# Performance work log

Hardware: AMD Instinct MI355X
Metric: run time of the kernel (lower is better)

## Reference

```python
import jax, jax.numpy as jnp
import numpy as np

EPS = 1e-5
TOPK = 4

def bn(x, gamma, beta, mean, var, axis=1):
    # inference-mode batchnorm (running stats)
    shp = [1] * x.ndim
    shp[axis] = -1
    scale = (gamma / jnp.sqrt(var + EPS)).reshape(shp)
    shift = (beta - mean * gamma / jnp.sqrt(var + EPS)).reshape(shp)
    return x * scale + shift


def setup_inputs() -> dict:
    key = jax.random.key(0)
    ks = jax.random.split(key, 4)
    B, C, T, H, W = 8, 512, 8, 28, 28
    R = 64
    Cq = C // 4
    s = 0.05
    return {
        "input": jax.random.normal(ks[0], (B, C, T, H, W), dtype=jnp.float32),
        "w_reduce": jax.random.normal(ks[1], (R, C), dtype=jnp.float32) * s,
        "bn1_gamma": jnp.ones((R,), jnp.float32), "bn1_beta": jnp.zeros((R,), jnp.float32),
        "bn1_mean": jnp.zeros((R,), jnp.float32), "bn1_var": jnp.ones((R,), jnp.float32),
        "w_proj": jax.random.normal(ks[2], (Cq, C + 2), dtype=jnp.float32) * s,
        "bn2_gamma": jnp.ones((Cq,), jnp.float32), "bn2_beta": jnp.zeros((Cq,), jnp.float32),
        "bn2_mean": jnp.zeros((Cq,), jnp.float32), "bn2_var": jnp.ones((Cq,), jnp.float32),
        "w_t": jax.random.normal(ks[3], (C, Cq, 3, 1), dtype=jnp.float32) * s,
        "bn3_gamma": jnp.ones((C,), jnp.float32), "bn3_beta": jnp.zeros((C,), jnp.float32),
        "bn3_mean": jnp.zeros((C,), jnp.float32), "bn3_var": jnp.ones((C,), jnp.float32),
    }


def reference(input, w_reduce, bn1_gamma, bn1_beta, bn1_mean, bn1_var,
              w_proj, bn2_gamma, bn2_beta, bn2_mean, bn2_var,
              w_t, bn3_gamma, bn3_beta, bn3_mean, bn3_var):
    x = input
    B, C, T, H, W = x.shape
    R = w_reduce.shape[0]
    K = TOPK
    HW = H * W

    # spatial template from frame 0
    template_d = x[:, :, 0].reshape(B, C, HW)                                  # (B,C,HW)
    template_p = bn(jnp.einsum('rc,bcs->brs', w_reduce, template_d),
                    bn1_gamma, bn1_beta, bn1_mean, bn1_var)                     # (B,R,HW)
    spt_inds = jnp.argmax(template_p, axis=2)                                  # (B,R)
    template_resample = jnp.take_along_axis(template_d, spt_inds[:, None, :], axis=2)  # (B,C,R)

    x_flat = x.reshape(B, C, T * HW)
    affinity = jnp.einsum('bcr,bcs->brs', template_resample, x_flat)           # (B,R,T*HW)
    affinity = affinity.reshape(B, R, T, HW)
    _, topk_inds = jax.lax.top_k(affinity, K)                                  # (B,R,T,K)
    inds = jnp.transpose(topk_inds, (0, 3, 2, 1))                              # (B,K,T,R)

    # gather trajectory features: traj[b,k,c,t,r] = x[b,c,t, inds[b,k,t,r]]
    x4 = x.reshape(B, C, T, HW)
    traj = jnp.take_along_axis(x4[:, None], inds[:, :, None], axis=4)          # (B,K,C,T,R)
    traj_bk = traj.reshape(B * K, C, T, R)

    inds_bk = inds.reshape(B * K, 1, T, R)
    row = (inds_bk // W).astype(jnp.float32) / H
    col = (inds_bk % W).astype(jnp.float32) / W
    coords = jnp.concatenate([row, col], axis=1)                               # (B*K,2,T,R)

    fuse = jnp.concatenate([traj_bk, coords], axis=1)                          # (B*K,C+2,T,R)
    fuse = bn(jnp.einsum('qc,bctr->bqtr', w_proj, fuse),
              bn2_gamma, bn2_beta, bn2_mean, bn2_var)                          # (B*K,C/4,T,R)
    fuse = fuse.reshape(B, K, C // 4, T, R).max(axis=1)                        # (B,C/4,T,R)

    tc = jax.lax.conv_general_dilated(fuse, w_t, window_strides=(1, 1),
                                      padding=((1, 1), (0, 0)),
                                      dimension_numbers=('NCHW', 'OIHW', 'NCHW'))
    tc = jax.nn.relu(bn(tc, bn3_gamma, bn3_beta, bn3_mean, bn3_var))           # (B,C,T,R)

    points = traj.mean(axis=1).reshape(B, C, T * R)                            # (B,C,T*R)
    proj = jnp.einsum('bcp,bcs->bps', points, x_flat)                          # (B,T*R,T*HW)
    proj = jax.nn.softmax(proj, axis=1)                                        # softmax over T*R (dim=1)
    prop = jnp.einsum('bcp,bps->bcs', tc.reshape(B, C, T * R), proj)           # (B,C,T*HW)
    return x + prop.reshape(B, C, T, H, W)
```

## Files before the change

### kernel.cpp

```cpp
#include <hip/hip_runtime.h>

#define EPSB 1e-5f

#define B_   8
#define C_   512
#define T_   8
#define HW_  784
#define S_   6272
#define R_   64
#define CQ_  128
#define K_   4
#define P_   512

typedef _Float16 f16;
typedef __attribute__((ext_vector_type(8))) _Float16 f16x8;
typedef __attribute__((ext_vector_type(4))) _Float16 f16x4;
typedef __attribute__((ext_vector_type(4))) float    f32x4;

#define OB_PTST  0ull
#define OB_TC    4194304ull
#define OB_D     8388608ull
#define OB_TRH   8589312ull
#define OB_TRF   9113600ull
#define OB_INDS  10162176ull
#define OB_WRH   10227712ull
#define OB_WPH   10293248ull
#define OB_WTH   10424320ull
#define OB_XT    10817536ull
#define T_TPA    62197760ull
#define T_AFF    63803392ull
#define T_FUSEK  62197760ull
#define T_FUSE   66392064ull
#define CHB      62197760ull

__device__ __forceinline__ void gload16(const void* g, void* l) {
    __builtin_amdgcn_global_load_lds(
        (const __attribute__((address_space(1))) unsigned int*)g,
        (__attribute__((address_space(3))) unsigned int*)l, 16, 0, 0);
}

__global__ __launch_bounds__(256) void k_prep(
    const float* __restrict__ wr, const float* __restrict__ wp,
    const float* __restrict__ wt,
    f16* __restrict__ wrh, f16* __restrict__ wph, f16* __restrict__ wth)
{
    int i = blockIdx.x*256 + threadIdx.x;
    if (i < 32768) {
        wrh[i] = (f16)wr[i];
    } else if (i < 98304) {
        int j = i - 32768;
        int q = j >> 9, c = j & 511;
        wph[j] = (f16)wp[q*514 + c];
    } else {
        int j = i - 98304;
        int co = j / 384;
        int rem = j - co*384;
        int dt = rem >> 7, ci = rem & 127;
        wth[j] = (f16)wt[(size_t)(co*CQ_ + ci)*3 + dt];
    }
}

__global__ __launch_bounds__(256) void k_xpose(
    const float* __restrict__ x, f16* __restrict__ xT)
{
    __shared__ float tile[64][65];
    int s0 = blockIdx.x*64, c0 = blockIdx.y*64, b = blockIdx.z;
    int tid = threadIdx.x;
    #pragma unroll
    for (int i = 0; i < 4; ++i) {
        int idx = tid + i*256;
        int cl = idx >> 4, s4 = (idx & 15)*4;
        f32x4 v = *(const f32x4*)&x[((size_t)(b*C_ + c0+cl))*S_ + s0 + s4];
        tile[cl][s4] = v.x; tile[cl][s4+1] = v.y;
        tile[cl][s4+2] = v.z; tile[cl][s4+3] = v.w;
    }
    __syncthreads();
    #pragma unroll
    for (int i = 0; i < 4; ++i) {
        int idx = tid + i*256;
        int sl = idx >> 4, c4 = (idx & 15)*4;
        f16x4 h;
        h[0] = (f16)tile[c4+0][sl]; h[1] = (f16)tile[c4+1][sl];
        h[2] = (f16)tile[c4+2][sl]; h[3] = (f16)tile[c4+3][sl];
        *(f16x4*)&xT[((size_t)(b*S_ + s0+sl))*C_ + c0 + c4] = h;
    }
}

__global__ __launch_bounds__(256) void k_templ(
    const f16* __restrict__ xT, const f16* __restrict__ wrh,
    float* __restrict__ tpa)
{
    __shared__ __align__(16) f16 As[128*64];
    __shared__ __align__(16) f16 Bs[64*64];
    int b = blockIdx.y; int s0 = blockIdx.x*128;
    int tid = threadIdx.x;
    int lane = tid & 63, w = tid >> 6;
    int lrow = lane >> 3;
    int swzc = ((lane & 7) ^ lrow) * 8;
    const f16* ga = xT  + ((size_t)b*S_ + s0 + w*32 + lrow)*C_ + swzc;
    const f16* gb = wrh + (size_t)(w*16 + lrow)*C_ + swzc;
    int mbase = (w & 1)*64, nbase = (w >> 1)*32;
    int fr = lane & 15, quad = lane >> 4;
    int sw = fr & 7;
    f32x4 acc[4][2] = {};
    for (int c0 = 0; c0 < C_; c0 += 64) {
        #pragma unroll
        for (int j = 0; j < 4; ++j)
            gload16(ga + j*8*C_, &As[(w*32 + j*8)*64]);
        #pragma unroll
        for (int j = 0; j < 2; ++j)
            gload16(gb + j*8*C_, &Bs[(w*16 + j*8)*64]);
        ga += 64; gb += 64;
        __syncthreads();
        #pragma unroll
        for (int kk = 0; kk < 2; ++kk) {
            int ch = ((kk*4 + quad) ^ sw) * 8;
            f16x8 af[4], bf[2];
            #pragma unroll
            for (int mt = 0; mt < 4; ++mt)
                af[mt] = *(const f16x8*)&As[(mbase + mt*16 + fr)*64 + ch];
            #pragma unroll
            for (int nt = 0; nt < 2; ++nt)
                bf[nt] = *(const f16x8*)&Bs[(nbase + nt*16 + fr)*64 + ch];
            #pragma unroll
            for (int mt = 0; mt < 4; ++mt)
                #pragma unroll
                for (int nt = 0; nt < 2; ++nt)
                    acc[mt][nt] = __builtin_amdgcn_mfma_f32_16x16x32_f16(
                        af[mt], bf[nt], acc[mt][nt], 0, 0, 0);
        }
        __syncthreads();
    }
    #pragma unroll
    for (int mt = 0; mt < 4; ++mt) {
        int sb = s0 + mbase + mt*16 + quad*4;
        if (sb < HW_) {
            #pragma unroll
            for (int nt = 0; nt < 2; ++nt) {
                int r = nbase + nt*16 + fr;
                *(f32x4*)&tpa[((size_t)(b*R_ + r))*HW_ + sb] = acc[mt][nt];
            }
        }
    }
}

__global__ __launch_bounds__(256) void k_targmax(
    const float* __restrict__ x, const float* __restrict__ wr_g,
    const float* __restrict__ g1, const float* __restrict__ v1,
    const float* __restrict__ tpa,
    float* __restrict__ trf, f16* __restrict__ trh)
{
    __shared__ float row[HW_];
    __shared__ float sval[256];
    __shared__ int   sidx[256];
    __shared__ float cval[4];
    __shared__ int   cidx[4];
    __shared__ float eval_[4];
    __shared__ int   bestind;
    int bid = blockIdx.x;
    int b = bid >> 6, r = bid & 63;
    int tid = threadIdx.x;
    float sc = g1[r] * rsqrtf(v1[r] + EPSB);
    const float* tprow = tpa + (size_t)bid*HW_;
    for (int s = tid; s < HW_; s += 256) row[s] = tprow[s]*sc;
    __syncthreads();
    for (int pass = 0; pass < 4; ++pass) {
        float best = -INFINITY; int bi = 0;
        for (int s = tid; s < HW_; s += 256) {
            float v = row[s];
            if (v > best) { best = v; bi = s; }
        }
        sval[tid] = best; sidx[tid] = bi;
        __syncthreads();
        for (int off = 128; off > 0; off >>= 1) {
            if (tid < off) {
                float ov = sval[tid+off]; int oi = sidx[tid+off];
                if (ov > sval[tid] || (ov == sval[tid] && oi < sidx[tid])) {
                    sval[tid] = ov; sidx[tid] = oi;
                }
            }
            __syncthreads();
        }
        if (tid == 0) {
            cval[pass] = sval[0]; cidx[pass] = sidx[0];
            row[sidx[0]] = -INFINITY;
        }
        __syncthreads();
    }
    float thr = 0.05f * fabsf(sc);
    if (cval[0] - cval[1] >= thr) {
        if (tid == 0) bestind = cidx[0];
    } else {
        int w = tid >> 6, lane = tid & 63;
        int cand = cidx[w];
        float sum = 0.f;
        #pragma unroll
        for (int i = 0; i < 8; ++i) {
            int c = lane + i*64;
            sum += wr_g[r*C_ + c] * x[((size_t)(b*C_ + c))*S_ + cand];
        }
        #pragma unroll
        for (int off = 32; off > 0; off >>= 1) sum += __shfl_xor(sum, off);
        if (lane == 0) eval_[w] = sum*sc;
        __syncthreads();
        if (tid == 0) {
            float bv = eval_[0]; int bi2 = cidx[0];
            for (int j = 1; j < 4; ++j) {
                float v = eval_[j]; int ii = cidx[j];
                if (v > bv || (v == bv && ii < bi2)) { bv = v; bi2 = ii; }
            }
            bestind = bi2;
        }
    }
    __syncthreads();
    int ind = bestind;
    for (int c = tid; c < C_; c += 256) {
        float v = x[((size_t)(b*C_ + c))*S_ + ind];
        trf[(size_t)bid*C_ + c] = v;
        trh[(size_t)bid*C_ + c] = (f16)v;
    }
}

__global__ __launch_bounds__(256) void k_affin(
    const f16* __restrict__ xT, const f16* __restrict__ trh,
    float* __restrict__ aff)
{
    __shared__ __align__(16) f16 As[2][128*64];
    __shared__ __align__(16) f16 Bs[2][64*64];
    int b = blockIdx.y; int s0 = blockIdx.x*128;
    int tid = threadIdx.x;
    int lane = tid & 63, w = tid >> 6;
    int lrow = lane >> 3;
    int swzc = ((lane & 7) ^ lrow) * 8;
    const f16* ga = xT  + ((size_t)b*S_ + s0 + w*32 + lrow)*C_ + swzc;
    const f16* gb = trh + ((size_t)(b*R_) + w*16 + lrow)*C_ + swzc;
    int mbase = (w & 1)*64, nbase = (w >> 1)*32;
    int fr = lane & 15, quad = lane >> 4;
    int sw = fr & 7;
    f32x4 acc[4][2] = {};
    #pragma unroll
    for (int j = 0; j < 4; ++j)
        gload16(ga + j*8*C_, &As[0][(w*32 + j*8)*64]);
    #pragma unroll
    for (int j = 0; j < 2; ++j)
        gload16(gb + j*8*C_, &Bs[0][(w*16 + j*8)*64]);
    ga += 64; gb += 64;
    __syncthreads();
    int cur = 0;
    for (int c0 = 0; c0 < C_; c0 += 64) {
        if (c0 + 64 < C_) {
            #pragma unroll
            for (int j = 0; j < 4; ++j)
                gload16(ga + j*8*C_, &As[cur^1][(w*32 + j*8)*64]);
            #pragma unroll
            for (int j = 0; j < 2; ++j)
                gload16(gb + j*8*C_, &Bs[cur^1][(w*16 + j*8)*64]);
            ga += 64; gb += 64;
        }
        #pragma unroll
        for (int kk = 0; kk < 2; ++kk) {
            int ch = ((kk*4 + quad) ^ sw) * 8;
            f16x8 af[4], bf[2];
            #pragma unroll
            for (int mt = 0; mt < 4; ++mt)
                af[mt] = *(const f16x8*)&As[cur][(mbase + mt*16 + fr)*64 + ch];
            #pragma unroll
            for (int nt = 0; nt < 2; ++nt)
                bf[nt] = *(const f16x8*)&Bs[cur][(nbase + nt*16 + fr)*64 + ch];
            #pragma unroll
            for (int mt = 0; mt < 4; ++mt)
                #pragma unroll
                for (int nt = 0; nt < 2; ++nt)
                    acc[mt][nt] = __builtin_amdgcn_mfma_f32_16x16x32_f16(
                        af[mt], bf[nt], acc[mt][nt], 0, 0, 0);
        }
        __syncthreads();
        cur ^= 1;
    }
    #pragma unroll
    for (int mt = 0; mt < 4; ++mt) {
        int sb = s0 + mbase + mt*16 + quad*4;
        #pragma unroll
        for (int nt = 0; nt < 2; ++nt) {
            int r = nbase + nt*16 + fr;
            *(f32x4*)&aff[((size_t)(b*R_ + r))*S_ + sb] = acc[mt][nt];
        }
    }
}

__global__ __launch_bounds__(256) void k_topk(
    const float* __restrict__ x, const float* __restrict__ trf,
    const float* __restrict__ aff, int* __restrict__ inds)
{
    __shared__ float row[HW_];
    __shared__ float sval[256];
    __shared__ int   sidx[256];
    __shared__ float cval[8];
    __shared__ int   cidx[8];
    __shared__ float eval_[8];
    int r = blockIdx.x, t = blockIdx.y, b = blockIdx.z;
    int tid = threadIdx.x;
    const float* arow = aff + ((size_t)(b*R_ + r))*S_ + t*HW_;
    for (int s = tid; s < HW_; s += 256) row[s] = arow[s];
    __syncthreads();
    for (int pass = 0; pass < 8; ++pass) {
        float best = -INFINITY; int bi = 0;
        for (int s = tid; s < HW_; s += 256) {
            float v = row[s];
            if (v > best) { best = v; bi = s; }
        }
        sval[tid] = best; sidx[tid] = bi;
        __syncthreads();
        for (int off = 128; off > 0; off >>= 1) {
            if (tid < off) {
                float ov = sval[tid+off]; int oi = sidx[tid+off];
                if (ov > sval[tid] || (ov == sval[tid] && oi < sidx[tid])) {
                    sval[tid] = ov; sidx[tid] = oi;
                }
            }
            __syncthreads();
        }
        if (tid == 0) {
            cval[pass] = sval[0]; cidx[pass] = sidx[0];
            row[sidx[0]] = -INFINITY;
        }
        __syncthreads();
    }
    if (cval[3] - cval[4] >= 0.35f) {
        if (tid < K_)
            inds[((b*K_ + tid)*T_ + t)*R_ + r] = cidx[tid];
    } else {
        int w = tid >> 6, lane = tid & 63;
        #pragma unroll
        for (int half = 0; half < 2; ++half) {
            int j = w + half*4;
            int cand = cidx[j];
            float sum = 0.f;
            #pragma unroll
            for (int i = 0; i < 8; ++i) {
                int c = lane + i*64;
                sum += trf[((size_t)(b*R_ + r))*C_ + c]
                     * x[((size_t)(b*C_ + c))*S_ + t*HW_ + cand];
            }
            #pragma unroll
            for (int off = 32; off > 0; off >>= 1) sum += __shfl_xor(sum, off);
            if (lane == 0) eval_[j] = sum;
        }
        __syncthreads();
        if (tid == 0) {
            unsigned used = 0;
            for (int k = 0; k < K_; ++k) {
                float bv = -INFINITY; int bj = -1;
                for (int j = 0; j < 8; ++j) {
                    if (used & (1u << j)) continue;
                    float v = eval_[j]; int ii = cidx[j];
                    if (bj < 0 || v > bv || (v == bv && ii < cidx[bj])) {
                        bv = v; bj = j;
                    }
                }
                used |= 1u << bj;
                inds[((b*K_ + k)*T_ + t)*R_ + r] = cidx[bj];
            }
        }
    }
}

__global__ __launch_bounds__(256) void k_pointsT(
    const float* __restrict__ x, const int* __restrict__ inds,
    f16* __restrict__ ptsT)
{
    __shared__ float tile[64][65];
    __shared__ int   indl[4][64];
    int c0 = blockIdx.x*64, t = blockIdx.y, b = blockIdx.z;
    int tid = threadIdx.x;
    {
        int k = tid >> 6, r = tid & 63;
        indl[k][r] = inds[((b*K_ + k)*T_ + t)*R_ + r];
    }
    __syncthreads();
    #pragma unroll
    for (int i = 0; i < 16; ++i) {
        int idx = tid + i*256;
        int cl = idx >> 6, r = idx & 63;
        const float* base = x + (size_t)(b*C_ + c0 + cl)*S_ + t*HW_;
        float v = base[indl[0][r]] + base[indl[1][r]] + base[indl[2][r]] + base[indl[3][r]];
        tile[cl][r] = 0.25f*v;
    }
    __syncthreads();
    #pragma unroll
    for (int i = 0; i < 16; ++i) {
        int idx = tid + i*256;
        int rl = idx >> 6, cl = idx & 63;
        ptsT[((size_t)b*P_ + t*64 + rl)*C_ + c0 + cl] = (f16)tile[cl][rl];
    }
}

__global__ __launch_bounds__(256) void k_fuse(
    const f16* __restrict__ xT, const f16* __restrict__ wph,
    const float* __restrict__ wp,
    const float* __restrict__ g2, const float* __restrict__ b2,
    const float* __restrict__ m2, const float* __restrict__ v2,
    f16* __restrict__ fusekT, const int* __restrict__ inds)
{
    __shared__ __align__(16) f16 As[128*32];
    __shared__ __align__(16) f16 Bs[64*32];
    __shared__ float scq[128], shq[128], wrq[128], wcq[128];
    __shared__ float rowv[64], colv[64];
    int bid = blockIdx.x;
    int t = bid & 7, bk = bid >> 3;
    int b = bk >> 2;
    int tid = threadIdx.x;
    int lane = tid & 63, w = tid >> 6;
    if (tid < 128) {
        float sc = g2[tid] * rsqrtf(v2[tid] + EPSB);
        scq[tid] = sc;
        shq[tid] = b2[tid] - m2[tid]*sc;
        wrq[tid] = wp[tid*514 + 512];
        wcq[tid] = wp[tid*514 + 513];
    } else if (tid < 192) {
        int r = tid - 128;
        int id = inds[bk*T_*R_ + t*R_ + r];
        rowv[r] = (float)(id / 28) * (1.0f/28.0f);
        colv[r] = (float)(id % 28) * (1.0f/28.0f);
    }
    int srow = w*16 + (lane >> 2);
    int scol = (lane & 3)*8;
    int ind = inds[bk*T_*R_ + t*R_ + srow];
    const f16* ga = wph + (size_t)srow*C_ + scol;
    const f16* gb = xT + ((size_t)b*S_ + t*HW_ + ind)*C_ + scol;
    int mbase = (w & 1)*64, nbase = (w >> 1)*32;
    int fr = lane & 15, fk = (lane >> 4)*8, quad = lane >> 4;
    f32x4 acc[4][2] = {};
    for (int c0 = 0; c0 < C_; c0 += 32) {
        gload16(ga,         &As[w*512]);
        gload16(ga + 64*C_, &As[2048 + w*512]);
        gload16(gb,         &Bs[w*512]);
        ga += 32; gb += 32;
        __syncthreads();
        f16x8 af[4], bf[2];
        #pragma unroll
        for (int mt = 0; mt < 4; ++mt)
            af[mt] = *(const f16x8*)&As[(mbase + mt*16 + fr)*32 + fk];
        #pragma unroll
        for (int nt = 0; nt < 2; ++nt)
            bf[nt] = *(const f16x8*)&Bs[(nbase + nt*16 + fr)*32 + fk];
        #pragma unroll
        for (int mt = 0; mt < 4; ++mt)
            #pragma unroll
            for (int nt = 0; nt < 2; ++nt)
                acc[mt][nt] = __builtin_amdgcn_mfma_f32_16x16x32_f16(
                    af[mt], bf[nt], acc[mt][nt], 0, 0, 0);
        __syncthreads();
    }
    #pragma unroll
    for (int mt = 0; mt < 4; ++mt) {
        int qb = mbase + mt*16 + quad*4;
        #pragma unroll
        for (int nt = 0; nt < 2; ++nt) {
            int r = nbase + nt*16 + fr;
            f16x4 h;
            #pragma unroll
            for (int i = 0; i < 4; ++i) {
                int q = qb + i;
                float v = acc[mt][nt][i] + wrq[q]*rowv[r] + wcq[q]*colv[r];
                h[i] = (f16)(v*scq[q] + shq[q]);
            }
            *(f16x4*)&fusekT[((size_t)bk*P_ + t*R_ + r)*CQ_ + qb] = h;
        }
    }
}

__global__ __launch_bounds__(256) void k_maxk(
    const f16* __restrict__ fusekT, f16* __restrict__ fuseT)
{
    int idx8 = (blockIdx.x*256 + threadIdx.x)*8;
    int b = idx8 >> 16;
    int pq = idx8 & 65535;
    const f16* base = fusekT + (size_t)(b*4)*65536 + pq;
    f16x8 v0 = *(const f16x8*)base;
    #pragma unroll
    for (int k = 1; k < K_; ++k) {
        f16x8 vk = *(const f16x8*)(base + (size_t)k*65536);
        #pragma unroll
        for (int j = 0; j < 8; ++j)
            v0[j] = (float)vk[j] > (float)v0[j] ? vk[j] : v0[j];
    }
    *(f16x8*)&fuseT[(size_t)b*65536 + pq] = v0;
}

__global__ __launch_bounds__(256) void k_conv(
    const f16* __restrict__ wth,
    const float* __restrict__ g3, const float* __restrict__ b3,
    const float* __restrict__ m3, const float* __restrict__ v3,
    const f16* __restrict__ fuseT, f16* __restrict__ tc)
{
    __shared__ __align__(16) f16 As[128*64];
    __shared__ __align__(16) f16 Bs[128*64];
    int p0 = blockIdx.x*128, c0 = blockIdx.y*128, b = blockIdx.z;
    int tid = threadIdx.x;
    int lane = tid & 63, w = tid >> 6;
    int lrow = lane >> 3;
    int swzc = ((lane & 7) ^ lrow) * 8;
    int mrow = (w & 1)*64, nrow = (w >> 1)*64;
    int fr = lane & 15, quad = lane >> 4;
    int sw = fr & 7;
    f32x4 acc[4][4] = {};
    for (int step = 0; step < 6; ++step) {
        int dt = step >> 1, h = step & 1;
        int shift = (dt - 1)*64;
        #pragma unroll
        for (int j = 0; j < 4; ++j) {
            int rb = w*32 + j*8;
            int pg = p0 + rb + shift;
            if (pg >= 0 && pg < P_)
                gload16(fuseT + ((size_t)b*P_ + pg + lrow)*CQ_ + h*64 + swzc,
                        &As[rb*64]);
            else
                *(f32x4*)((char*)&As[rb*64] + lane*16) = (f32x4){0.f,0.f,0.f,0.f};
        }
        #pragma unroll
        for (int j = 0; j < 4; ++j) {
            int rb = w*32 + j*8;
            gload16(wth + (size_t)(c0 + rb + lrow)*384 + dt*128 + h*64 + swzc,
                    &Bs[rb*64]);
        }
        __syncthreads();
        #pragma unroll
        for (int kk = 0; kk < 2; ++kk) {
            int ch = ((kk*4 + quad) ^ sw) * 8;
            f16x8 af[4], bf[4];
            #pragma unroll
            for (int mt = 0; mt < 4; ++mt)
                af[mt] = *(const f16x8*)&As[(mrow + mt*16 + fr)*64 + ch];
            #pragma unroll
            for (int nt = 0; nt < 4; ++nt)
                bf[nt] = *(const f16x8*)&Bs[(nrow + nt*16 + fr)*64 + ch];
            #pragma unroll
            for (int mt = 0; mt < 4; ++mt)
                #pragma unroll
                for (int nt = 0; nt < 4; ++nt)
                    acc[mt][nt] = __builtin_amdgcn_mfma_f32_16x16x32_f16(
                        af[mt], bf[nt], acc[mt][nt], 0, 0, 0);
        }
        __syncthreads();
    }
    #pragma unroll
    for (int nt = 0; nt < 4; ++nt) {
        int co = c0 + nrow + nt*16 + fr;
        float sc = g3[co] * rsqrtf(v3[co] + EPSB);
        float sh = b3[co] - m3[co]*sc;
        #pragma unroll
        for (int mt = 0; mt < 4; ++mt) {
            int p = p0 + mrow + mt*16 + quad*4;
            f16x4 hv;
            #pragma unroll
            for (int i = 0; i < 4; ++i)
                hv[i] = (f16)fmaxf(acc[mt][nt][i]*sc + sh, 0.f);
            *(f16x4*)&tc[((size_t)(b*C_ + co))*P_ + p] = hv;
        }
    }
}

__global__ __launch_bounds__(512, 2) void k_attnW(
    const f16* __restrict__ xT, const f16* __restrict__ ptsT,
    f16* __restrict__ W, float* __restrict__ Dinv, int st, int NCHb)
{
    __shared__ __align__(16) f16 As[128*64];
    __shared__ __align__(16) f16 Bs[512*64];
    __shared__ float red[128][4];
    int lt = blockIdx.x; int b = blockIdx.z;
    int s0 = (st + lt)*128;
    int tid = threadIdx.x;
    int lane = tid & 63, w = tid >> 6;
    int wr = w & 1, wc = w >> 1;
    int lrow = lane >> 3;
    int swzc = ((lane & 7) ^ lrow) * 8;
    const f16* ga = xT   + ((size_t)b*S_ + s0 + w*16 + lrow)*C_ + swzc;
    const f16* gb = ptsT + ((size_t)b*P_ + w*64 + lrow)*C_ + swzc;
    int fr = lane & 15, quad = lane >> 4;
    int sw = fr & 7;
    f32x4 acc[8][4] = {};
    for (int c0 = 0; c0 < C_; c0 += 64) {
        #pragma unroll
        for (int j = 0; j < 2; ++j)
            gload16(ga + j*8*C_, &As[(w*16 + j*8)*64]);
        #pragma unroll
        for (int j = 0; j < 8; ++j)
            gload16(gb + j*8*C_, &Bs[(w*64 + j*8)*64]);
        ga += 64; gb += 64;
        __syncthreads();
        #pragma unroll
        for (int kk = 0; kk < 2; ++kk) {
            int ch = ((kk*4 + quad) ^ sw) * 8;
            f16x8 af[4], bf[8];
            #pragma unroll
            for (int mt = 0; mt < 4; ++mt)
                af[mt] = *(const f16x8*)&As[(wr*64 + mt*16 + fr)*64 + ch];
            #pragma unroll
            for (int nt = 0; nt < 8; ++nt)
                bf[nt] = *(const f16x8*)&Bs[(wc*128 + nt*16 + fr)*64 + ch];
            #pragma unroll
            for (int nt = 0; nt < 8; ++nt)
                #pragma unroll
                for (int mt = 0; mt < 4; ++mt)
                    acc[nt][mt] = __builtin_amdgcn_mfma_f32_16x16x32_f16(
                        bf[nt], af[mt], acc[nt][mt], 0, 0, 0);
        }
        __syncthreads();
    }
    float M[4];
    #pragma unroll
    for (int mt = 0; mt < 4; ++mt) {
        float m = -INFINITY;
        #pragma unroll
        for (int nt = 0; nt < 8; ++nt)
            #pragma unroll
            for (int i = 0; i < 4; ++i)
                m = fmaxf(m, acc[nt][mt][i]);
        m = fmaxf(m, __shfl_xor(m, 16));
        m = fmaxf(m, __shfl_xor(m, 32));
        if (quad == 0) red[wr*64 + mt*16 + fr][wc] = m;
    }
    __syncthreads();
    #pragma unroll
    for (int mt = 0; mt < 4; ++mt) {
        int srow = wr*64 + mt*16 + fr;
        M[mt] = fmaxf(fmaxf(red[srow][0], red[srow][1]),
                      fmaxf(red[srow][2], red[srow][3]));
    }
    __syncthreads();
    #pragma unroll
    for (int mt = 0; mt < 4; ++mt) {
        float s = 0.f;
        #pragma unroll
        for (int nt = 0; nt < 8; ++nt)
            #pragma unroll
            for (int i = 0; i < 4; ++i) {
                float e = __expf(acc[nt][mt][i] - M[mt]);
                acc[nt][mt][i] = e;
                s += e;
            }
        s += __shfl_xor(s, 16);
        s += __shfl_xor(s, 32);
        if (quad == 0) red[wr*64 + mt*16 + fr][wc] = s;
    }
    __syncthreads();
    size_t wbase = (size_t)(b*NCHb + lt)*128*(size_t)P_;
    #pragma unroll
    for (int mt = 0; mt < 4; ++mt) {
        int srow = wr*64 + mt*16 + fr;
        float tot = (red[srow][0] + red[srow][1]) + (red[srow][2] + red[srow][3]);
        if (wc == 0 && quad == 0)
            Dinv[(size_t)b*S_ + s0 + srow] = 1.0f/tot;
        #pragma unroll
        for (int nt = 0; nt < 8; ++nt) {
            f16x4 h;
            #pragma unroll
            for (int i = 0; i < 4; ++i) h[i] = (f16)acc[nt][mt][i];
            *(f16x4*)&W[wbase + (size_t)srow*P_ + wc*128 + nt*16 + quad*4] = h;
        }
    }
}

__global__ __launch_bounds__(256) void k_gemmP(
    const f16* __restrict__ tc, const f16* __restrict__ W,
    const float* __restrict__ Dinv, const float* __restrict__ x,
    float* __restrict__ out, int st, int NCHb)
{
    __shared__ __align__(16) f16 As[2][128*64];
    __shared__ __align__(16) f16 Bs[2][128*64];
    int lt = blockIdx.x; int b = blockIdx.z;
    int s0 = (st + lt)*128, c0t = blockIdx.y*128;
    int tid = threadIdx.x;
    int lane = tid & 63, w = tid >> 6;
    int lrow = lane >> 3;
    int swzc = ((lane & 7) ^ lrow) * 8;
    const f16* ga = tc + ((size_t)(b*C_) + c0t + w*32 + lrow)*P_ + swzc;
    const f16* gb = W  + ((size_t)(b*NCHb + lt)*128 + w*32 + lrow)*P_ + swzc;
    int mrow = (w & 1)*64, nrow = (w >> 1)*64;
    int fr = lane & 15, quad = lane >> 4;
    int sw = fr & 7;
    f32x4 acc[4][4] = {};
    #pragma unroll
    for (int j = 0; j < 4; ++j)
        gload16(ga + j*8*P_, &As[0][(w*32 + j*8)*64]);
    #pragma unroll
    for (int j = 0; j < 4; ++j)
        gload16(gb + j*8*P_, &Bs[0][(w*32 + j*8)*64]);
    ga += 64; gb += 64;
    __syncthreads();
    int cur = 0;
    for (int p0 = 0; p0 < P_; p0 += 64) {
        if (p0 + 64 < P_) {
            #pragma unroll
            for (int j = 0; j < 4; ++j)
                gload16(ga + j*8*P_, &As[cur^1][(w*32 + j*8)*64]);
            #pragma unroll
            for (int j = 0; j < 4; ++j)
                gload16(gb + j*8*P_, &Bs[cur^1][(w*32 + j*8)*64]);
            ga += 64; gb += 64;
        }
        #pragma unroll
        for (int kk = 0; kk < 2; ++kk) {
            int ch = ((kk*4 + quad) ^ sw) * 8;
            f16x8 af[4], bf[4];
            #pragma unroll
            for (int mt = 0; mt < 4; ++mt)
                af[mt] = *(const f16x8*)&As[cur][(mrow + mt*16 + fr)*64 + ch];
            #pragma unroll
            for (int nt = 0; nt < 4; ++nt)
                bf[nt] = *(const f16x8*)&Bs[cur][(nrow + nt*16 + fr)*64 + ch];
            #pragma unroll
            for (int nt = 0; nt < 4; ++nt)
                #pragma unroll
                for (int mt = 0; mt < 4; ++mt)
                    acc[nt][mt] = __builtin_amdgcn_mfma_f32_16x16x32_f16(
                        bf[nt], af[mt], acc[nt][mt], 0, 0, 0);
        }
        __syncthreads();
        cur ^= 1;
    }
    #pragma unroll
    for (int nt = 0; nt < 4; ++nt) {
        int s = s0 + nrow + nt*16 + quad*4;
        f32x4 dv = *(const f32x4*)&Dinv[(size_t)b*S_ + s];
        #pragma unroll
        for (int mt = 0; mt < 4; ++mt) {
            int c = c0t + mrow + mt*16 + fr;
            size_t o = ((size_t)(b*C_ + c))*S_ + s;
            f32x4 xv = *(const f32x4*)&x[o];
            f32x4 res = xv + acc[nt][mt]*dv;
            *(f32x4*)&out[o] = res;
        }
    }
}

extern "C" void kernel_launch(void* const* d_in, const int* in_sizes, int n_in,
                              void* d_out, int out_size, void* d_ws, size_t ws_size,
                              hipStream_t stream) {
    const float* x   = (const float*)d_in[0];
    const float* wrd = (const float*)d_in[1];
    const float* g1  = (const float*)d_in[2];
    const float* v1  = (const float*)d_in[5];
    const float* wp  = (const float*)d_in[6];
    const float* g2  = (const float*)d_in[7];
    const float* b2  = (const float*)d_in[8];
    const float* m2  = (const float*)d_in[9];
    const float* v2  = (const float*)d_in[10];
    const float* wt  = (const float*)d_in[11];
    const float* g3  = (const float*)d_in[12];
    const float* b3  = (const float*)d_in[13];
    const float* m3  = (const float*)d_in[14];
    const float* v3  = (const float*)d_in[15];
    char*  wsb = (char*)d_ws;
    float* out = (float*)d_out;

    f16*   ptsT  = (f16*)  (wsb + OB_PTST);
    f16*   tc    = (f16*)  (wsb + OB_TC);
    float* Dinv  = (float*)(wsb + OB_D);
    f16*   trh   = (f16*)  (wsb + OB_TRH);
    float* trf   = (float*)(wsb + OB_TRF);
    int*   inds  = (int*)  (wsb + OB_INDS);
    f16*   wrh   = (f16*)  (wsb + OB_WRH);
    f16*   wph   = (f16*)  (wsb + OB_WPH);
    f16*   wth   = (f16*)  (wsb + OB_WTH);
    f16*   xT    = (f16*)  (wsb + OB_XT);
    float* tpa   = (float*)(wsb + T_TPA);
    float* aff   = (float*)(wsb + T_AFF);
    f16*   fusekT= (f16*)  (wsb + T_FUSEK);
    f16*   fuseT = (f16*)  (wsb + T_FUSE);

    const size_t PER_TILE = 1048576ull;
    size_t avail = ws_size > CHB ? ws_size - CHB : 0;
    int NCH = (int)(avail / PER_TILE);
    if (NCH < 1) NCH = 1;
    if (NCH > 49) NCH = 49;
    int nchunks = (49 + NCH - 1)/NCH;
    int NCHb = (49 + nchunks - 1)/nchunks;
    f16* W = (f16*)(wsb + CHB);

    k_prep<<<1152, 256, 0, stream>>>(wrd, wp, wt, wrh, wph, wth);
    k_xpose<<<dim3(98, 8, 8), 256, 0, stream>>>(x, xT);
    k_templ<<<dim3(7, 8), 256, 0, stream>>>(xT, wrh, tpa);
    k_targmax<<<512, 256, 0, stream>>>(x, wrd, g1, v1, tpa, trf, trh);
    k_affin<<<dim3(49, 8), 256, 0, stream>>>(xT, trh, aff);
    k_topk<<<dim3(R_, T_, B_), 256, 0, stream>>>(x, trf, aff, inds);
    k_pointsT<<<dim3(8, 8, 8), 256, 0, stream>>>(x, inds, ptsT);
    k_fuse<<<256, 256, 0, stream>>>(xT, wph, wp, g2, b2, m2, v2, fusekT, inds);
    k_maxk<<<256, 256, 0, stream>>>(fusekT, fuseT);
    k_conv<<<dim3(4, 4, 8), 256, 0, stream>>>(wth, g3, b3, m3, v3, fuseT, tc);

    for (int st = 0; st < 49; st += NCHb) {
        int cnt = (49 - st) < NCHb ? (49 - st) : NCHb;
        k_attnW<<<dim3(cnt, 1, 8), 512, 0, stream>>>(xT, ptsT, W, Dinv, st, NCHb);
        k_gemmP<<<dim3(cnt, 4, 8), 256, 0, stream>>>(tc, W, Dinv, x, out, st, NCHb);
    }
}
```

Baseline: 484.5 us.

## Double-buffer GEMM LDS tiles with partial vmcnt waits across all MFMA kernels

Converts the template, affinity, fuse, projection and output GEMM kernels to a double-buffered global_load_lds pipeline. Each iteration prefetches the next tile, then waits only for the current tile's loads with a partial s_waitcnt vmcnt and a raw s_barrier instead of __syncthreads. The fuse and projection kernels also move to 32-wide K slices with an XOR swizzle, and the projection kernel reuses As as its reduction scratch to keep LDS within budget. The hand-set vmcnt counts must match the number of issued loads exactly, otherwise a race appears.

```diff
diff --git a/kernel.cpp b/kernel.cpp
--- a/kernel.cpp
+++ b/kernel.cpp
@@ -33,6 +33,10 @@
 #define T_FUSE   66392064ull
 #define CHB      62197760ull
 
+#define SBAR()  __builtin_amdgcn_s_barrier()
+#define SCHB()  __builtin_amdgcn_sched_barrier(0)
+#define WAITV(N) asm volatile("s_waitcnt vmcnt(" #N ")" ::: "memory")
+
 __device__ __forceinline__ void gload16(const void* g, void* l) {
     __builtin_amdgcn_global_load_lds(
         (const __attribute__((address_space(1))) unsigned int*)g,
@@ -90,8 +94,8 @@
     const f16* __restrict__ xT, const f16* __restrict__ wrh,
     float* __restrict__ tpa)
 {
-    __shared__ __align__(16) f16 As[128*64];
-    __shared__ __align__(16) f16 Bs[64*64];
+    __shared__ __align__(16) f16 As[2][128*64];
+    __shared__ __align__(16) f16 Bs[2][64*64];
     int b = blockIdx.y; int s0 = blockIdx.x*128;
     int tid = threadIdx.x;
     int lane = tid & 63, w = tid >> 6;
@@ -103,25 +107,38 @@
     int fr = lane & 15, quad = lane >> 4;
     int sw = fr & 7;
     f32x4 acc[4][2] = {};
-    for (int c0 = 0; c0 < C_; c0 += 64) {
-        #pragma unroll
-        for (int j = 0; j < 4; ++j)
-            gload16(ga + j*8*C_, &As[(w*32 + j*8)*64]);
-        #pragma unroll
-        for (int j = 0; j < 2; ++j)
-            gload16(gb + j*8*C_, &Bs[(w*16 + j*8)*64]);
-        ga += 64; gb += 64;
-        __syncthreads();
+    #pragma unroll
+    for (int j = 0; j < 4; ++j)
+        gload16(ga + j*8*C_, &As[0][(w*32 + j*8)*64]);
+    #pragma unroll
+    for (int j = 0; j < 2; ++j)
+        gload16(gb + j*8*C_, &Bs[0][(w*16 + j*8)*64]);
+    ga += 64; gb += 64;
+    int cur = 0;
+    for (int i = 0; i < 8; ++i) {
+        if (i < 7) {
+            #pragma unroll
+            for (int j = 0; j < 4; ++j)
+                gload16(ga + j*8*C_, &As[cur^1][(w*32 + j*8)*64]);
+            #pragma unroll
+            for (int j = 0; j < 2; ++j)
+                gload16(gb + j*8*C_, &Bs[cur^1][(w*16 + j*8)*64]);
+            ga += 64; gb += 64;
+            WAITV(6);
+        } else {
+            WAITV(0);
+        }
+        SCHB(); SBAR();
         #pragma unroll
         for (int kk = 0; kk < 2; ++kk) {
             int ch = ((kk*4 + quad) ^ sw) * 8;
             f16x8 af[4], bf[2];
             #pragma unroll
             for (int mt = 0; mt < 4; ++mt)
-                af[mt] = *(const f16x8*)&As[(mbase + mt*16 + fr)*64 + ch];
+                af[mt] = *(const f16x8*)&As[cur][(mbase + mt*16 + fr)*64 + ch];
             #pragma unroll
             for (int nt = 0; nt < 2; ++nt)
-                bf[nt] = *(const f16x8*)&Bs[(nbase + nt*16 + fr)*64 + ch];
+                bf[nt] = *(const f16x8*)&Bs[cur][(nbase + nt*16 + fr)*64 + ch];
             #pragma unroll
             for (int mt = 0; mt < 4; ++mt)
                 #pragma unroll
@@ -129,7 +146,8 @@
                     acc[mt][nt] = __builtin_amdgcn_mfma_f32_16x16x32_f16(
                         af[mt], bf[nt], acc[mt][nt], 0, 0, 0);
         }
-        __syncthreads();
+        SBAR();
+        cur ^= 1;
     }
     #pragma unroll
     for (int mt = 0; mt < 4; ++mt) {
@@ -245,10 +263,9 @@
     for (int j = 0; j < 2; ++j)
         gload16(gb + j*8*C_, &Bs[0][(w*16 + j*8)*64]);
     ga += 64; gb += 64;
-    __syncthreads();
     int cur = 0;
-    for (int c0 = 0; c0 < C_; c0 += 64) {
-        if (c0 + 64 < C_) {
+    for (int i = 0; i < 8; ++i) {
+        if (i < 7) {
             #pragma unroll
             for (int j = 0; j < 4; ++j)
                 gload16(ga + j*8*C_, &As[cur^1][(w*32 + j*8)*64]);
@@ -256,7 +273,11 @@
             for (int j = 0; j < 2; ++j)
                 gload16(gb + j*8*C_, &Bs[cur^1][(w*16 + j*8)*64]);
             ga += 64; gb += 64;
-        }
+            WAITV(6);
+        } else {
+            WAITV(0);
+        }
+        SCHB(); SBAR();
         #pragma unroll
         for (int kk = 0; kk < 2; ++kk) {
             int ch = ((kk*4 + quad) ^ sw) * 8;
@@ -274,7 +295,7 @@
                     acc[mt][nt] = __builtin_amdgcn_mfma_f32_16x16x32_f16(
                         af[mt], bf[nt], acc[mt][nt], 0, 0, 0);
         }
-        __syncthreads();
+        SBAR();
         cur ^= 1;
     }
     #pragma unroll
@@ -402,8 +423,8 @@
     const float* __restrict__ m2, const float* __restrict__ v2,
     f16* __restrict__ fusekT, const int* __restrict__ inds)
 {
-    __shared__ __align__(16) f16 As[128*32];
-    __shared__ __align__(16) f16 Bs[64*32];
+    __shared__ __align__(16) f16 As[2][128*32];
+    __shared__ __align__(16) f16 Bs[2][64*32];
     __shared__ float scq[128], shq[128], wrq[128], wcq[128];
     __shared__ float rowv[64], colv[64];
     int bid = blockIdx.x;
@@ -423,34 +444,50 @@
         rowv[r] = (float)(id / 28) * (1.0f/28.0f);
         colv[r] = (float)(id % 28) * (1.0f/28.0f);
     }
-    int srow = w*16 + (lane >> 2);
-    int scol = (lane & 3)*8;
-    int ind = inds[bk*T_*R_ + t*R_ + srow];
-    const f16* ga = wph + (size_t)srow*C_ + scol;
-    const f16* gb = xT + ((size_t)b*S_ + t*HW_ + ind)*C_ + scol;
+    int strow = tid >> 2;
+    int slot  = (tid & 3) ^ (strow & 3);
+    int ind = inds[bk*T_*R_ + t*R_ + strow];
+    const f16* ga = wph + (size_t)strow*C_ + slot*8;
+    const f16* gb = xT + ((size_t)b*S_ + t*HW_ + ind)*C_ + slot*8;
     int mbase = (w & 1)*64, nbase = (w >> 1)*32;
-    int fr = lane & 15, fk = (lane >> 4)*8, quad = lane >> 4;
+    int fr = lane & 15, quad = lane >> 4;
     f32x4 acc[4][2] = {};
-    for (int c0 = 0; c0 < C_; c0 += 32) {
-        gload16(ga,         &As[w*512]);
-        gload16(ga + 64*C_, &As[2048 + w*512]);
-        gload16(gb,         &Bs[w*512]);
-        ga += 32; gb += 32;
-        __syncthreads();
+    __syncthreads();
+    gload16(ga,         (f16*)As[0] + tid*8);
+    gload16(ga + 64*C_, (f16*)As[0] + 2048 + tid*8);
+    gload16(gb,         (f16*)Bs[0] + tid*8);
+    ga += 32; gb += 32;
+    int cur = 0;
+    for (int i = 0; i < 16; ++i) {
+        if (i < 15) {
+            gload16(ga,         (f16*)As[cur^1] + tid*8);
+            gload16(ga + 64*C_, (f16*)As[cur^1] + 2048 + tid*8);
+            gload16(gb,         (f16*)Bs[cur^1] + tid*8);
+            ga += 32; gb += 32;
+            WAITV(3);
+        } else {
+            WAITV(0);
+        }
+        SCHB(); SBAR();
         f16x8 af[4], bf[2];
         #pragma unroll
-        for (int mt = 0; mt < 4; ++mt)
-            af[mt] = *(const f16x8*)&As[(mbase + mt*16 + fr)*32 + fk];
-        #pragma unroll
-        for (int nt = 0; nt < 2; ++nt)
-            bf[nt] = *(const f16x8*)&Bs[(nbase + nt*16 + fr)*32 + fk];
+        for (int mt = 0; mt < 4; ++mt) {
+            int ar = mbase + mt*16 + fr;
+            af[mt] = *(const f16x8*)&As[cur][ar*32 + ((quad ^ (ar & 3))*8)];
+        }
+        #pragma unroll
+        for (int nt = 0; nt < 2; ++nt) {
+            int br = nbase + nt*16 + fr;
+            bf[nt] = *(const f16x8*)&Bs[cur][br*32 + ((quad ^ (br & 3))*8)];
+        }
         #pragma unroll
         for (int mt = 0; mt < 4; ++mt)
             #pragma unroll
             for (int nt = 0; nt < 2; ++nt)
                 acc[mt][nt] = __builtin_amdgcn_mfma_f32_16x16x32_f16(
                     af[mt], bf[nt], acc[mt][nt], 0, 0, 0);
-        __syncthreads();
+        SBAR();
+        cur ^= 1;
     }
     #pragma unroll
     for (int mt = 0; mt < 4; ++mt) {
@@ -565,49 +602,58 @@
     const f16* __restrict__ xT, const f16* __restrict__ ptsT,
     f16* __restrict__ W, float* __restrict__ Dinv, int st, int NCHb)
 {
-    __shared__ __align__(16) f16 As[128*64];
-    __shared__ __align__(16) f16 Bs[512*64];
-    __shared__ float red[128][4];
+    __shared__ __align__(16) f16 As[2][128*32];
+    __shared__ __align__(16) f16 Bs[2][512*32];
     int lt = blockIdx.x; int b = blockIdx.z;
     int s0 = (st + lt)*128;
     int tid = threadIdx.x;
     int lane = tid & 63, w = tid >> 6;
     int wr = w & 1, wc = w >> 1;
-    int lrow = lane >> 3;
-    int swzc = ((lane & 7) ^ lrow) * 8;
-    const f16* ga = xT   + ((size_t)b*S_ + s0 + w*16 + lrow)*C_ + swzc;
-    const f16* gb = ptsT + ((size_t)b*P_ + w*64 + lrow)*C_ + swzc;
+    int strow = tid >> 2;
+    int slot  = (tid & 3) ^ (strow & 3);
+    const f16* ga = xT   + ((size_t)b*S_ + s0 + strow)*C_ + slot*8;
+    const f16* gb = ptsT + ((size_t)b*P_ + strow)*C_ + slot*8;
     int fr = lane & 15, quad = lane >> 4;
-    int sw = fr & 7;
     f32x4 acc[8][4] = {};
-    for (int c0 = 0; c0 < C_; c0 += 64) {
-        #pragma unroll
-        for (int j = 0; j < 2; ++j)
-            gload16(ga + j*8*C_, &As[(w*16 + j*8)*64]);
-        #pragma unroll
-        for (int j = 0; j < 8; ++j)
-            gload16(gb + j*8*C_, &Bs[(w*64 + j*8)*64]);
-        ga += 64; gb += 64;
-        __syncthreads();
-        #pragma unroll
-        for (int kk = 0; kk < 2; ++kk) {
-            int ch = ((kk*4 + quad) ^ sw) * 8;
-            f16x8 af[4], bf[8];
+    gload16(ga, (f16*)As[0] + tid*8);
+    #pragma unroll
+    for (int j = 0; j < 4; ++j)
+        gload16(gb + (size_t)j*128*C_, (f16*)Bs[0] + j*4096 + tid*8);
+    ga += 32; gb += 32;
+    int cur = 0;
+    for (int i = 0; i < 16; ++i) {
+        if (i < 15) {
+            gload16(ga, (f16*)As[cur^1] + tid*8);
+            #pragma unroll
+            for (int j = 0; j < 4; ++j)
+                gload16(gb + (size_t)j*128*C_, (f16*)Bs[cur^1] + j*4096 + tid*8);
+            ga += 32; gb += 32;
+            WAITV(5);
+        } else {
+            WAITV(0);
+        }
+        SCHB(); SBAR();
+        f16x8 af[4], bf[8];
+        #pragma unroll
+        for (int mt = 0; mt < 4; ++mt) {
+            int ar = wr*64 + mt*16 + fr;
+            af[mt] = *(const f16x8*)&As[cur][ar*32 + ((quad ^ (ar & 3))*8)];
+        }
+        #pragma unroll
+        for (int nt = 0; nt < 8; ++nt) {
+            int br = wc*128 + nt*16 + fr;
+            bf[nt] = *(const f16x8*)&Bs[cur][br*32 + ((quad ^ (br & 3))*8)];
+        }
+        #pragma unroll
+        for (int nt = 0; nt < 8; ++nt)
             #pragma unroll
             for (int mt = 0; mt < 4; ++mt)
-                af[mt] = *(const f16x8*)&As[(wr*64 + mt*16 + fr)*64 + ch];
-            #pragma unroll
-            for (int nt = 0; nt < 8; ++nt)
-                bf[nt] = *(const f16x8*)&Bs[(wc*128 + nt*16 + fr)*64 + ch];
-            #pragma unroll
-            for (int nt = 0; nt < 8; ++nt)
-                #pragma unroll
-                for (int mt = 0; mt < 4; ++mt)
-                    acc[nt][mt] = __builtin_amdgcn_mfma_f32_16x16x32_f16(
-                        bf[nt], af[mt], acc[nt][mt], 0, 0, 0);
-        }
-        __syncthreads();
-    }
+                acc[nt][mt] = __builtin_amdgcn_mfma_f32_16x16x32_f16(
+                    bf[nt], af[mt], acc[nt][mt], 0, 0, 0);
+        SBAR();
+        cur ^= 1;
+    }
+    float (*red)[4] = (float (*)[4])As;
     float M[4];
     #pragma unroll
     for (int mt = 0; mt < 4; ++mt) {
@@ -688,10 +734,9 @@
     for (int j = 0; j < 4; ++j)
         gload16(gb + j*8*P_, &Bs[0][(w*32 + j*8)*64]);
     ga += 64; gb += 64;
-    __syncthreads();
     int cur = 0;
-    for (int p0 = 0; p0 < P_; p0 += 64) {
-        if (p0 + 64 < P_) {
+    for (int i = 0; i < 8; ++i) {
+        if (i < 7) {
             #pragma unroll
             for (int j = 0; j < 4; ++j)
                 gload16(ga + j*8*P_, &As[cur^1][(w*32 + j*8)*64]);
@@ -699,7 +744,11 @@
             for (int j = 0; j < 4; ++j)
                 gload16(gb + j*8*P_, &Bs[cur^1][(w*32 + j*8)*64]);
             ga += 64; gb += 64;
-        }
+            WAITV(8);
+        } else {
+            WAITV(0);
+        }
+        SCHB(); SBAR();
         #pragma unroll
         for (int kk = 0; kk < 2; ++kk) {
             int ch = ((kk*4 + quad) ^ sw) * 8;
@@ -717,7 +766,7 @@
                     acc[nt][mt] = __builtin_amdgcn_mfma_f32_16x16x32_f16(
                         bf[nt], af[mt], acc[nt][mt], 0, 0, 0);
         }
-        __syncthreads();
+        SBAR();
         cur ^= 1;
     }
     #pragma unroll
```

Result: no change. 480.4 us (-0.8%).
